# Kernel tuning notes

Measured on AMD Instinct MI355X. Metric: run time of the kernel, lower is better.

## Reference

```python
import jax, jax.numpy as jnp
import numpy as np

TEMPERATURE = 0.6
REPETITION_PENALTY = 1.2
VOCAB = 50257


def setup_inputs() -> dict:
    key = jax.random.key(0)
    k1, k2 = jax.random.split(key)
    logits = jax.random.normal(k1, (8, 64, VOCAB), dtype=jnp.float32)
    prev_tokens = jax.random.randint(k2, (64, 200), 0, VOCAB, dtype=jnp.int64)
    return {"logits": logits, "prev_tokens": prev_tokens}


def reference(logits, prev_tokens):
    # logits: [B, S, V]; prev_tokens: [S, P] token ids previously generated per sequence.
    B, S, V = logits.shape
    # set-semantics mask of penalized (seq, token) pairs; duplicate ids collapse to one.
    mask = jnp.zeros((S, V), dtype=bool).at[
        jnp.arange(S)[:, None], prev_tokens
    ].set(True)  # [S, V]
    # torch.all over dim 0: penalty multiplies if all batch logits negative, else divides.
    all_neg = jnp.all(logits < 0, axis=0, keepdims=True)  # [1, S, V]
    penalized = jnp.where(all_neg, logits * REPETITION_PENALTY, logits / REPETITION_PENALTY)
    logits = jnp.where(mask[None, :, :], penalized, logits)
    # Categorical(logits=x) -> probs = softmax(x); temperature scaling fused.
    return jax.nn.softmax(logits / TEMPERATURE, axis=-1)
```

## Files before the change

### kernel.cpp

```cpp
#include <hip/hip_runtime.h>
#include <math.h>

#define BB 8
#define SS 64
#define VV 50257
#define PP 200
#define NMASK 1571
#define NT 1024
#define ITER 13
constexpr float RP   = 1.2f;
constexpr float TINV = 1.0f / 0.6f;

typedef float f32x4 __attribute__((ext_vector_type(4)));

__global__ __launch_bounds__(NT) void sch_fused_kernel(
        const float* __restrict__ logits,
        const int*   __restrict__ prev,
        float*       __restrict__ out) {
    __shared__ unsigned mask[NMASK];
    __shared__ float ss[16];
    __shared__ float bc_li;

    const int bs  = blockIdx.x;
    const int s   = bs & (SS - 1);
    const int tid = threadIdx.x;
    const float* row  = logits + (size_t)bs * VV;
    float*       orow = out    + (size_t)bs * VV;

    const int a0   = (4 - (bs & 3)) & 3;
    const int nb   = (VV - a0) >> 2;
    const int tail = VV - a0 - (nb << 2);
    const int tstart = a0 + (nb << 2);
    const f32x4* body = (const f32x4*)(row + a0);
    const bool has_head = (tid < a0);
    const bool has_tail = (tid >= 4 && tid < 4 + tail);

    int   vtok = -1;
    float lv[BB];
    if (tid < PP) {
        vtok = prev[s * PP + tid];
        #pragma unroll
        for (int b = 0; b < BB; ++b)
            lv[b] = logits[((size_t)(b * SS + s)) * VV + vtok];
    }
    for (int i = tid; i < NMASK; i += NT) mask[i] = 0u;
    __syncthreads();

    bool winner = false;
    if (tid < PP) {
        unsigned bit = 1u << (vtok & 31);
        unsigned old = atomicOr(&mask[vtok >> 5], bit);
        winner = (old & bit) == 0u;
    }

    float accx = 0.f, accy = 0.f, accz = 0.f, accw = 0.f;
    #pragma unroll
    for (int k = 0; k < ITER; ++k) {
        int i = tid + k * NT;
        if (i < nb) {
            f32x4 x = body[i];
            accx += __expf(x.x * TINV);
            accy += __expf(x.y * TINV);
            accz += __expf(x.z * TINV);
            accw += __expf(x.w * TINV);
        }
    }
    float sum = (accx + accy) + (accz + accw);
    if (has_head) sum += __expf(row[tid] * TINV);
    if (has_tail) sum += __expf(row[tstart + tid - 4] * TINV);

    float eadj = 0.0f;
    if (winner) {
        bool all_neg = true;
        #pragma unroll
        for (int b = 0; b < BB; ++b) all_neg = all_neg && (lv[b] < 0.0f);
        const float myraw = lv[bs >> 6];
        const float adj   = all_neg ? myraw * RP : myraw / RP;
        eadj = __expf(adj * TINV);
        sum += eadj - __expf(myraw * TINV);
    }

    #pragma unroll
    for (int off = 1; off < 64; off <<= 1)
        sum += __shfl_xor(sum, off);
    const int wave = tid >> 6, lane = tid & 63;
    if (lane == 0) ss[wave] = sum;
    __syncthreads();
    if (tid == 0) {
        float S0 = ss[0];
        #pragma unroll
        for (int w = 1; w < 16; ++w) S0 += ss[w];
        bc_li = 1.0f / S0;
    }
    __syncthreads();
    const float li = bc_li;

    f32x4* obody = (f32x4*)(orow + a0);
    #pragma unroll
    for (int k = 0; k < ITER; ++k) {
        int i = tid + k * NT;
        if (i < nb) {
            f32x4 x = body[i];
            f32x4 o;
            o.x = __expf(x.x * TINV) * li;
            o.y = __expf(x.y * TINV) * li;
            o.z = __expf(x.z * TINV) * li;
            o.w = __expf(x.w * TINV) * li;
            __builtin_nontemporal_store(o, &obody[i]);
        }
    }
    if (has_head)
        __builtin_nontemporal_store(__expf(row[tid] * TINV) * li, &orow[tid]);
    if (has_tail)
        __builtin_nontemporal_store(__expf(row[tstart + tid - 4] * TINV) * li,
                                    &orow[tstart + tid - 4]);

    __syncthreads();
    if (winner) orow[vtok] = eadj * li;
}

extern "C" void kernel_launch(void* const* d_in, const int* in_sizes, int n_in,
                              void* d_out, int out_size, void* d_ws, size_t ws_size,
                              hipStream_t stream) {
    const float* logits = (const float*)d_in[0];
    const int*   prev   = (const int*)d_in[1];
    float* out = (float*)d_out;

    sch_fused_kernel<<<BB * SS, NT, 0, stream>>>(logits, prev, out);
}
```

Baseline: 202.8 us.

## Split fused softmax into two kernels with chunked rows and precomputed penalty bitmasks

Replaces the single 1024-thread-per-row kernel with two launches. The first computes per-row partial exp-sums over four chunks, plus per-sequence penalty and all-negative bitmasks and sum corrections. The second rescales each element using the bitmasks and normalizes. This gives many more, smaller blocks (2048 plus 64) to raise parallelism and occupancy. In exchange it adds a second kernel launch, a workspace dependency, and extra bitmask reads, and it swaps the nontemporal stores in the fallback for regular stores.

```diff
diff --git a/kernel.cpp b/kernel.cpp
--- a/kernel.cpp
+++ b/kernel.cpp
@@ -5,13 +5,173 @@
 #define SS 64
 #define VV 50257
 #define PP 200
+#define NW 1571
+#define CH 4
+#define NT2 256
+#define IT2 13
+#define NBQ (NT2 * IT2)
+constexpr float RP   = 1.2f;
+constexpr float RPI  = 1.0f / 1.2f;
+constexpr float TINV = 1.0f / 0.6f;
+constexpr float RPT  = RP * TINV;
+constexpr float RPIT = RPI * TINV;
+
+typedef float f32x4 __attribute__((ext_vector_type(4)));
+
+
+__device__ __forceinline__ float scale1(float x, int v, const uint2* brow,
+                                        float li) {
+    uint2 c = brow[v >> 5];
+    unsigned sh = (unsigned)v & 31u;
+    bool bit = (c.x >> sh) & 1u;
+    bool ab  = (c.y >> sh) & 1u;
+    float f = bit ? (ab ? RPT : RPIT) : TINV;
+    return __expf(x * f) * li;
+}
+
+__global__ __launch_bounds__(NT2) void k_sum(
+        const float* __restrict__ logits,
+        const int*   __restrict__ prev,
+        float*       __restrict__ wsum,
+        uint2*       __restrict__ bits) {
+    const int blk = blockIdx.x;
+    const int tid = threadIdx.x;
+
+    __shared__ unsigned lmask[NW];
+    __shared__ unsigned lall[NW];
+    __shared__ float    dsum[BB];
+    __shared__ float    wpart[NT2 / 64];
+
+    if (blk < SS) {
+        const int s = blk;
+        for (int i = tid; i < NW; i += NT2) { lmask[i] = 0u; lall[i] = 0u; }
+        if (tid < BB) dsum[tid] = 0.f;
+        __syncthreads();
+
+        if (tid < PP) {
+            int tok = prev[s * PP + tid];
+            unsigned bit = 1u << (tok & 31);
+            unsigned old = atomicOr(&lmask[tok >> 5], bit);
+            if (!(old & bit)) {
+                float lv[BB];
+                bool alln = true;
+                #pragma unroll
+                for (int b = 0; b < BB; ++b) {
+                    lv[b] = logits[((size_t)(b * SS + s)) * VV + tok];
+                    alln = alln && (lv[b] < 0.f);
+                }
+                if (alln) atomicOr(&lall[tok >> 5], bit);
+                const float ft = alln ? RPT : RPIT;
+                #pragma unroll
+                for (int b = 0; b < BB; ++b) {
+                    float d = __expf(lv[b] * ft) - __expf(lv[b] * TINV);
+                    atomicAdd(&dsum[b], d);
+                }
+            }
+        }
+        __syncthreads();
+
+        uint2* brow = bits + (size_t)s * NW;
+        for (int i = tid; i < NW; i += NT2)
+            brow[i] = make_uint2(lmask[i], lall[i]);
+        if (tid < BB) wsum[(tid * SS + s) * 8 + 4] = dsum[tid];
+        return;
+    }
+
+    const int cblk  = blk - SS;
+    const int row   = cblk >> 2;
+    const int chunk = cblk & 3;
+    const int a0 = (4 - (row & 3)) & 3;
+    const int nb = (VV - a0) >> 2;
+    const float* rowp = logits + (size_t)row * VV;
+    const f32x4* body = (const f32x4*)(rowp + a0);
+
+    float acc = 0.f;
+    #pragma unroll
+    for (int k = 0; k < IT2; ++k) {
+        int fi = chunk * NBQ + k * NT2 + tid;
+        if (fi < nb) {
+            f32x4 x = body[fi];
+            acc += __expf(x.x * TINV) + __expf(x.y * TINV)
+                 + __expf(x.z * TINV) + __expf(x.w * TINV);
+        }
+    }
+    if (chunk == 0) {
+        const int tail   = VV - a0 - (nb << 2);
+        const int tstart = a0 + (nb << 2);
+        if (tid < a0)                 acc += __expf(rowp[tid] * TINV);
+        if (tid >= 4 && tid < 4 + tail)
+            acc += __expf(rowp[tstart + tid - 4] * TINV);
+    }
+    #pragma unroll
+    for (int off = 1; off < 64; off <<= 1) acc += __shfl_xor(acc, off);
+    const int wave = tid >> 6, lane = tid & 63;
+    if (lane == 0) wpart[wave] = acc;
+    __syncthreads();
+    if (tid == 0)
+        wsum[row * 8 + chunk] = (wpart[0] + wpart[1]) + (wpart[2] + wpart[3]);
+}
+
+__global__ __launch_bounds__(NT2) void k_scale(
+        const float* __restrict__ logits,
+        const float* __restrict__ wsum,
+        const uint2* __restrict__ bits,
+        float*       __restrict__ out) {
+    const int blk   = blockIdx.x;
+    const int tid   = threadIdx.x;
+    const int row   = blk >> 2;
+    const int chunk = blk & 3;
+    const int s     = row & (SS - 1);
+    const int a0 = (4 - (row & 3)) & 3;
+    const int nb = (VV - a0) >> 2;
+    const float* rowp = logits + (size_t)row * VV;
+    float*       orow = out    + (size_t)row * VV;
+    const f32x4* body  = (const f32x4*)(rowp + a0);
+    f32x4*       obody = (f32x4*)(orow + a0);
+    const uint2* brow  = bits + (size_t)s * NW;
+
+    const float* wr = wsum + row * 8;
+    const float S  = ((wr[0] + wr[1]) + (wr[2] + wr[3])) + wr[4];
+    const float li = 1.0f / S;
+
+    #pragma unroll
+    for (int k = 0; k < IT2; ++k) {
+        int fi = chunk * NBQ + k * NT2 + tid;
+        if (fi < nb) {
+            f32x4 x = body[fi];
+            const int vb = a0 + (fi << 2);
+            const int w0 = vb >> 5, w3 = (vb + 3) >> 5;
+            uint2 c0 = brow[w0];
+            uint2 c3 = brow[w3];
+            f32x4 o;
+            #pragma unroll
+            for (int j = 0; j < 4; ++j) {
+                const int v = vb + j;
+                uint2 c = ((v >> 5) == w0) ? c0 : c3;
+                unsigned sh = (unsigned)v & 31u;
+                bool bit = (c.x >> sh) & 1u;
+                bool ab  = (c.y >> sh) & 1u;
+                float f = bit ? (ab ? RPT : RPIT) : TINV;
+                o[j] = __expf(x[j] * f) * li;
+            }
+            obody[fi] = o;
+        }
+    }
+    if (chunk == 0) {
+        const int tail   = VV - a0 - (nb << 2);
+        const int tstart = a0 + (nb << 2);
+        if (tid < a0)
+            orow[tid] = scale1(rowp[tid], tid, brow, li);
+        if (tid >= 4 && tid < 4 + tail) {
+            int v = tstart + tid - 4;
+            orow[v] = scale1(rowp[v], v, brow, li);
+        }
+    }
+}
+
 #define NMASK 1571
 #define NT 1024
 #define ITER 13
-constexpr float RP   = 1.2f;
-constexpr float TINV = 1.0f / 0.6f;
-
-typedef float f32x4 __attribute__((ext_vector_type(4)));
 
 __global__ __launch_bounds__(NT) void sch_fused_kernel(
         const float* __restrict__ logits,
@@ -81,8 +241,7 @@
     }
 
     #pragma unroll
-    for (int off = 1; off < 64; off <<= 1)
-        sum += __shfl_xor(sum, off);
+    for (int off = 1; off < 64; off <<= 1) sum += __shfl_xor(sum, off);
     const int wave = tid >> 6, lane = tid & 63;
     if (lane == 0) ss[wave] = sum;
     __syncthreads();
@@ -106,14 +265,11 @@
             o.y = __expf(x.y * TINV) * li;
             o.z = __expf(x.z * TINV) * li;
             o.w = __expf(x.w * TINV) * li;
-            __builtin_nontemporal_store(o, &obody[i]);
-        }
-    }
-    if (has_head)
-        __builtin_nontemporal_store(__expf(row[tid] * TINV) * li, &orow[tid]);
-    if (has_tail)
-        __builtin_nontemporal_store(__expf(row[tstart + tid - 4] * TINV) * li,
-                                    &orow[tstart + tid - 4]);
+            obody[i] = o;
+        }
+    }
+    if (has_head) orow[tid]              = __expf(row[tid] * TINV) * li;
+    if (has_tail) orow[tstart + tid - 4] = __expf(row[tstart + tid - 4] * TINV) * li;
 
     __syncthreads();
     if (winner) orow[vtok] = eadj * li;
@@ -126,5 +282,13 @@
     const int*   prev   = (const int*)d_in[1];
     float* out = (float*)d_out;
 
-    sch_fused_kernel<<<BB * SS, NT, 0, stream>>>(logits, prev, out);
-}
+    const size_t need = 16384 + (size_t)SS * NW * sizeof(uint2);
+    if (d_ws != nullptr && ws_size >= need) {
+        float* wsum = (float*)d_ws;
+        uint2* bits = (uint2*)((char*)d_ws + 16384);
+        k_sum  <<<SS + BB * SS * CH, NT2, 0, stream>>>(logits, prev, wsum, bits);
+        k_scale<<<     BB * SS * CH, NT2, 0, stream>>>(logits, wsum, bits, out);
+    } else {
+        sch_fused_kernel<<<BB * SS, NT, 0, stream>>>(logits, prev, out);
+    }
+}
```

New measurement: 202.9 us. About the same (+0.1%).

## Shrink blocks to 256 threads and apply penalty via LDS bitmask in output pass

Applied to the files above, without the earlier changes.

Reduces the block size from 1024 to 256 threads, with 50 unrolled iterations per thread instead of 13. It replaces the post-write scatter fix-up, and the barrier before it, with a second LDS bitmask recording all-negative tokens. The output loop now selects a per-element exponent scale from the two bitmasks. This removes the trailing barrier and the scattered overwrite, but adds LDS reads and selects per vector, plus heavier per-thread unrolling that may raise register pressure.

```diff
diff --git a/kernel.cpp b/kernel.cpp
--- a/kernel.cpp
+++ b/kernel.cpp
@@ -5,118 +5,122 @@
 #define SS 64
 #define VV 50257
 #define PP 200
-#define NMASK 1571
-#define NT 1024
-#define ITER 13
+#define NW 1571
+#define NT 256
+#define IT 50
 constexpr float RP   = 1.2f;
+constexpr float RPI  = 1.0f / 1.2f;
 constexpr float TINV = 1.0f / 0.6f;
+constexpr float RPT  = RP * TINV;
+constexpr float RPIT = RPI * TINV;
 
 typedef float f32x4 __attribute__((ext_vector_type(4)));
 
-__global__ __launch_bounds__(NT) void sch_fused_kernel(
+
+__global__ __launch_bounds__(NT) void k_row(
         const float* __restrict__ logits,
         const int*   __restrict__ prev,
         float*       __restrict__ out) {
-    __shared__ unsigned mask[NMASK];
-    __shared__ float ss[16];
-    __shared__ float bc_li;
+    __shared__ unsigned lmask[NW];
+    __shared__ unsigned lall[NW];
+    __shared__ float    red[NT / 64];
+    __shared__ float    bcli;
 
     const int bs  = blockIdx.x;
     const int s   = bs & (SS - 1);
+    const int b   = bs >> 6;
     const int tid = threadIdx.x;
     const float* row  = logits + (size_t)bs * VV;
     float*       orow = out    + (size_t)bs * VV;
 
-    const int a0   = (4 - (bs & 3)) & 3;
-    const int nb   = (VV - a0) >> 2;
-    const int tail = VV - a0 - (nb << 2);
+    const int a0     = (4 - (bs & 3)) & 3;
+    const int nb     = (VV - a0) >> 2;
+    const int tail   = VV - a0 - (nb << 2);
     const int tstart = a0 + (nb << 2);
     const f32x4* body = (const f32x4*)(row + a0);
-    const bool has_head = (tid < a0);
-    const bool has_tail = (tid >= 4 && tid < 4 + tail);
+    const bool hh = (tid < a0);
+    const bool ht = (tid >= 4 && tid < 4 + tail);
+
+    for (int i = tid; i < NW; i += NT) { lmask[i] = 0u; lall[i] = 0u; }
+    __syncthreads();
 
     int   vtok = -1;
     float lv[BB];
     if (tid < PP) {
         vtok = prev[s * PP + tid];
         #pragma unroll
-        for (int b = 0; b < BB; ++b)
-            lv[b] = logits[((size_t)(b * SS + s)) * VV + vtok];
-    }
-    for (int i = tid; i < NMASK; i += NT) mask[i] = 0u;
-    __syncthreads();
-
-    bool winner = false;
-    if (tid < PP) {
-        unsigned bit = 1u << (vtok & 31);
-        unsigned old = atomicOr(&mask[vtok >> 5], bit);
-        winner = (old & bit) == 0u;
+        for (int j = 0; j < BB; ++j)
+            lv[j] = logits[((size_t)(j * SS + s)) * VV + vtok];
     }
 
-    float accx = 0.f, accy = 0.f, accz = 0.f, accw = 0.f;
+    float acc = 0.f;
     #pragma unroll
-    for (int k = 0; k < ITER; ++k) {
+    for (int k = 0; k < IT; ++k) {
         int i = tid + k * NT;
         if (i < nb) {
             f32x4 x = body[i];
-            accx += __expf(x.x * TINV);
-            accy += __expf(x.y * TINV);
-            accz += __expf(x.z * TINV);
-            accw += __expf(x.w * TINV);
+            acc += __expf(x.x * TINV) + __expf(x.y * TINV)
+                 + __expf(x.z * TINV) + __expf(x.w * TINV);
         }
     }
-    float sum = (accx + accy) + (accz + accw);
-    if (has_head) sum += __expf(row[tid] * TINV);
-    if (has_tail) sum += __expf(row[tstart + tid - 4] * TINV);
+    if (hh) acc += __expf(row[tid] * TINV);
+    if (ht) acc += __expf(row[tstart + tid - 4] * TINV);
 
-    float eadj = 0.0f;
-    if (winner) {
-        bool all_neg = true;
-        #pragma unroll
-        for (int b = 0; b < BB; ++b) all_neg = all_neg && (lv[b] < 0.0f);
-        const float myraw = lv[bs >> 6];
-        const float adj   = all_neg ? myraw * RP : myraw / RP;
-        eadj = __expf(adj * TINV);
-        sum += eadj - __expf(myraw * TINV);
+    if (tid < PP) {
+        unsigned bit = 1u << (vtok & 31);
+        unsigned old = atomicOr(&lmask[vtok >> 5], bit);
+        if (!(old & bit)) {
+            bool alln = true;
+            #pragma unroll
+            for (int j = 0; j < BB; ++j) alln = alln && (lv[j] < 0.f);
+            if (alln) atomicOr(&lall[vtok >> 5], bit);
+            const float ft = alln ? RPT : RPIT;
+            acc += __expf(lv[b] * ft) - __expf(lv[b] * TINV);
+        }
     }
 
     #pragma unroll
-    for (int off = 1; off < 64; off <<= 1)
-        sum += __shfl_xor(sum, off);
-    const int wave = tid >> 6, lane = tid & 63;
-    if (lane == 0) ss[wave] = sum;
+    for (int off = 1; off < 64; off <<= 1) acc += __shfl_xor(acc, off);
+    if ((tid & 63) == 0) red[tid >> 6] = acc;
     __syncthreads();
-    if (tid == 0) {
-        float S0 = ss[0];
-        #pragma unroll
-        for (int w = 1; w < 16; ++w) S0 += ss[w];
-        bc_li = 1.0f / S0;
-    }
+    if (tid == 0) bcli = 1.0f / ((red[0] + red[1]) + (red[2] + red[3]));
     __syncthreads();
-    const float li = bc_li;
+    const float li = bcli;
 
     f32x4* obody = (f32x4*)(orow + a0);
     #pragma unroll
-    for (int k = 0; k < ITER; ++k) {
+    for (int k = 0; k < IT; ++k) {
         int i = tid + k * NT;
         if (i < nb) {
             f32x4 x = body[i];
+            const int vb = a0 + (i << 2);
+            const int w0 = vb >> 5, w3 = (vb + 3) >> 5;
+            const unsigned m0 = lmask[w0], A0 = lall[w0];
+            const unsigned m3 = lmask[w3], A3 = lall[w3];
             f32x4 o;
-            o.x = __expf(x.x * TINV) * li;
-            o.y = __expf(x.y * TINV) * li;
-            o.z = __expf(x.z * TINV) * li;
-            o.w = __expf(x.w * TINV) * li;
+            #pragma unroll
+            for (int j = 0; j < 4; ++j) {
+                const int v = vb + j;
+                const unsigned mm = ((v >> 5) == w0) ? m0 : m3;
+                const unsigned aa = ((v >> 5) == w0) ? A0 : A3;
+                const unsigned sh = (unsigned)v & 31u;
+                const bool bit = (mm >> sh) & 1u;
+                const bool ab  = (aa >> sh) & 1u;
+                const float f  = bit ? (ab ? RPT : RPIT) : TINV;
+                o[j] = __expf(x[j] * f) * li;
+            }
             __builtin_nontemporal_store(o, &obody[i]);
         }
     }
-    if (has_head)
-        __builtin_nontemporal_store(__expf(row[tid] * TINV) * li, &orow[tid]);
-    if (has_tail)
-        __builtin_nontemporal_store(__expf(row[tstart + tid - 4] * TINV) * li,
-                                    &orow[tstart + tid - 4]);
-
-    __syncthreads();
-    if (winner) orow[vtok] = eadj * li;
+    if (hh || ht) {
+        const int v = hh ? tid : (tstart + tid - 4);
+        const unsigned mm = lmask[v >> 5], aa = lall[v >> 5];
+        const unsigned sh = (unsigned)v & 31u;
+        const bool bit = (mm >> sh) & 1u;
+        const bool ab  = (aa >> sh) & 1u;
+        const float f  = bit ? (ab ? RPT : RPIT) : TINV;
+        __builtin_nontemporal_store(__expf(row[v] * f) * li, &orow[v]);
+    }
 }
 
 extern "C" void kernel_launch(void* const* d_in, const int* in_sizes, int n_in,
@@ -126,5 +130,5 @@
     const int*   prev   = (const int*)d_in[1];
     float* out = (float*)d_out;
 
-    sch_fused_kernel<<<BB * SS, NT, 0, stream>>>(logits, prev, out);
+    k_row<<<BB * SS, NT, 0, stream>>>(logits, prev, out);
 }
```

Measured after the change: 198.1 us. 1.02x faster.
